# Optimization experiments

Hardware: AMD Instinct MI355X
Metric: run time of the kernel (lower is better)

The kernel has to match this reference:

```python
import jax, jax.numpy as jnp
import numpy as np

EPS = 1e-5

def conv_block(x, w, b, a, g, bt):
    # x: [B,Cin,T,F]; w: [Cout,Cin]; b: [Cout]; a: scalar PReLU slope; g,bt: [Cout,F]
    y = jnp.einsum('bctf,oc->botf', x, w) + b[None, :, None, None]
    y = jnp.maximum(y, 0.0) + a * jnp.minimum(y, 0.0)  # PReLU (single shared slope)
    mu = jnp.mean(y, axis=(1, 3), keepdims=True)
    var = jnp.var(y, axis=(1, 3), keepdims=True)       # unbiased=False
    y = (y - mu) / jnp.sqrt(var + EPS)
    return y * g[None, :, None, :] + bt[None, :, None, :]

# vmap over heads: weights have leading head axis, x is shared
_head_block = jax.vmap(conv_block, in_axes=(None, 0, 0, 0, 0, 0))


def setup_inputs() -> dict:
    key = jax.random.key(0)
    B, C, T, F = 8, 64, 1024, 64
    H, HID = 4, 4
    DV = C // H
    ks = jax.random.split(key, 16)
    s = 1.0 / np.sqrt(C)
    inp = {
        'x': jax.random.normal(ks[0], (B, C, T, F), jnp.float32),
        # per-head Q conv blocks
        'qw': jax.random.normal(ks[1], (H, HID, C), jnp.float32) * s,
        'qb': jax.random.normal(ks[2], (H, HID), jnp.float32) * 0.01,
        'qa': jnp.full((H,), 0.25, jnp.float32),
        'qg': jnp.ones((H, HID, F), jnp.float32),
        'qbeta': jnp.zeros((H, HID, F), jnp.float32),
        # per-head K conv blocks
        'kw': jax.random.normal(ks[3], (H, HID, C), jnp.float32) * s,
        'kb': jax.random.normal(ks[4], (H, HID), jnp.float32) * 0.01,
        'ka': jnp.full((H,), 0.25, jnp.float32),
        'kg': jnp.ones((H, HID, F), jnp.float32),
        'kbeta': jnp.zeros((H, HID, F), jnp.float32),
        # per-head V conv blocks (out = C//H)
        'vw': jax.random.normal(ks[5], (H, DV, C), jnp.float32) * s,
        'vb': jax.random.normal(ks[6], (H, DV), jnp.float32) * 0.01,
        'va': jnp.full((H,), 0.25, jnp.float32),
        'vg': jnp.ones((H, DV, F), jnp.float32),
        'vbeta': jnp.zeros((H, DV, F), jnp.float32),
        # final 'likear' conv block
        'lw': jax.random.normal(ks[7], (C, C), jnp.float32) * s,
        'lb': jax.random.normal(ks[8], (C,), jnp.float32) * 0.01,
        'la': jnp.float32(0.25),
        'lg': jnp.ones((C, F), jnp.float32),
        'lbeta': jnp.zeros((C, F), jnp.float32),
    }
    return inp


def reference(x, qw, qb, qa, qg, qbeta, kw, kb, ka, kg, kbeta,
              vw, vb, va, vg, vbeta, lw, lb, la, lg, lbeta):
    B, C, T, F = x.shape
    H = qw.shape[0]
    HID = qw.shape[1]
    DV = C // H
    embed = H * F  # embed_size = num_heads * num_freqs

    Q = _head_block(x, qw, qb, qa, qg, qbeta)  # [H,B,HID,T,F]
    K = _head_block(x, kw, kb, ka, kg, kbeta)  # [H,B,HID,T,F]
    V = _head_block(x, vw, vb, va, vg, vbeta)  # [H,B,DV,T,F]

    # cat over dim 0 == head-major reshape; transpose(1,2)+flatten(2)
    Ql = Q.reshape(H * B, HID, T, F).transpose(0, 2, 1, 3).reshape(H * B, T, HID * F)
    Kl = K.reshape(H * B, HID, T, F).transpose(0, 2, 1, 3).reshape(H * B, T, HID * F)
    Vl = V.reshape(H * B, DV, T, F).transpose(0, 2, 1, 3).reshape(H * B, T, DV * F)

    scores = jnp.einsum('ntd,nsd->nts', Ql, Kl) / jnp.sqrt(jnp.float32(embed))
    attn = jax.nn.softmax(scores, axis=-1)               # [HB,T,T]
    A = jnp.einsum('nts,nsd->ntd', attn, Vl)             # [HB,T,DV*F]

    A = A.reshape(H * B, T, DV, F).transpose(0, 2, 1, 3)  # [HB,DV,T,F]
    A = A.reshape(H, B, DV, T, F).transpose(1, 0, 2, 3, 4).reshape(B, C, T, F)

    out = conv_block(A, lw, lb, la, lg, lbeta)
    return out + x
```

## Files before the change

kernel.cpp:

```cpp
#include <hip/hip_runtime.h>

typedef unsigned short u16;
typedef __attribute__((ext_vector_type(8))) short short8;
typedef __attribute__((ext_vector_type(4))) float f32x4;

#define EPSV 1e-5f

__device__ __forceinline__ u16 f2bf(float f) {
    unsigned u = __float_as_uint(f);
    u += 0x7fffu + ((u >> 16) & 1u);
    return (u16)(u >> 16);
}

__device__ __forceinline__ f32x4 mfma_bf16(short8 a, short8 b, f32x4 c) {
    return __builtin_amdgcn_mfma_f32_16x16x32_bf16(a, b, c, 0, 0, 0);
}

__device__ __forceinline__ void gload_lds16(const void* g, void* l) {
    __builtin_amdgcn_global_load_lds((const __attribute__((address_space(1))) void*)g,
                                     (__attribute__((address_space(3))) void*)l, 16, 0, 0);
}

__global__ __launch_bounds__(256) void k_prep_qkv(const float* __restrict__ qw,
                                                  const float* __restrict__ kw,
                                                  const float* __restrict__ vw,
                                                  u16* __restrict__ wq)
{
    const int tid = threadIdx.x;
#pragma unroll
    for (int i = 0; i < 24; i++) {
        int idx = tid + i * 256;
        int row = idx >> 6;
        float wv = (row < 16) ? qw[idx] : ((row < 32) ? kw[idx - 1024] : vw[idx - 2048]);
        wq[idx] = f2bf(wv);
    }
}

__global__ __launch_bounds__(256) void k_prep_lw(const float* __restrict__ lw, u16* __restrict__ lwb)
{
    const int tid = threadIdx.x;
#pragma unroll
    for (int i = 0; i < 16; i++) {
        int idx = tid + i * 256;
        lwb[idx] = f2bf(lw[idx]);
    }
}

__global__ __launch_bounds__(256) void k_qkv(
    const float* __restrict__ x, const u16* __restrict__ wq,
    const float* __restrict__ qb, const float* __restrict__ qa,
    const float* __restrict__ qg, const float* __restrict__ qbt,
    const float* __restrict__ kb, const float* __restrict__ ka,
    const float* __restrict__ kg, const float* __restrict__ kbt,
    const float* __restrict__ vb, const float* __restrict__ va,
    const float* __restrict__ vg, const float* __restrict__ vbt,
    u16* __restrict__ Qb, u16* __restrict__ Kb, u16* __restrict__ Vb)
{
    __shared__ u16 xT[64][66];
    __shared__ float ys[96][66];
    __shared__ float bias_s[96], slope_s[96];

    const int tid = threadIdx.x, w = tid >> 6, lane = tid & 63;
    const int b = blockIdx.x >> 10, t = blockIdx.x & 1023;
    const int lc = lane & 15, grp = lane >> 4;

    if (tid < 96) {
        int row = tid; float bv, sv;
        if (row < 16)      { bv = qb[row];      sv = qa[row >> 2]; }
        else if (row < 32) { bv = kb[row - 16]; sv = ka[(row - 16) >> 2]; }
        else               { bv = vb[row - 32]; sv = va[(row - 32) >> 4]; }
        bias_s[row] = bv; slope_s[row] = sv;
    }
    const float* xbt = x + ((size_t)(b * 64) * 1024 + t) * 64;
#pragma unroll
    for (int k = 0; k < 4; k++) {
        int chunk = tid + k * 256;
        int c = chunk >> 4, q = chunk & 15;
        float4 v = *(const float4*)(xbt + (size_t)c * 65536 + q * 4);
        xT[q * 4 + 0][c] = f2bf(v.x);
        xT[q * 4 + 1][c] = f2bf(v.y);
        xT[q * 4 + 2][c] = f2bf(v.z);
        xT[q * 4 + 3][c] = f2bf(v.w);
    }
    __syncthreads();

#pragma unroll
    for (int i = 0; i < 6; i++) {
        int tile = w * 6 + i;
        int mt = tile >> 2, nt = tile & 3;
        f32x4 acc = {0.f, 0.f, 0.f, 0.f};
#pragma unroll
        for (int kt = 0; kt < 2; kt++) {
            short8 a  = *(const short8*)(wq + (mt * 16 + lc) * 64 + kt * 32 + grp * 8);
            short8 bf = *(const short8*)(&xT[nt * 16 + lc][kt * 32 + grp * 8]);
            acc = mfma_bf16(a, bf, acc);
        }
        int colf = nt * 16 + lc;
#pragma unroll
        for (int j = 0; j < 4; j++) {
            int row = mt * 16 + grp * 4 + j;
            float y = acc[j] + bias_s[row];
            float sl = slope_s[row];
            y = (y > 0.f) ? y : sl * y;
            ys[row][colf] = y;
        }
    }
    __syncthreads();

    const int h = w;
    {
        float v0[4]; float s = 0.f, ss = 0.f;
#pragma unroll
        for (int o = 0; o < 4; o++) { float y = ys[h * 4 + o][lane]; v0[o] = y; s += y; ss += y * y; }
#pragma unroll
        for (int m = 1; m < 64; m <<= 1) { s += __shfl_xor(s, m, 64); ss += __shfl_xor(ss, m, 64); }
        float mu = s * (1.f / 256.f), var = ss * (1.f / 256.f) - mu * mu;
        float rs = rsqrtf(var + EPSV);
        size_t base = ((size_t)(h * 8 + b) * 1024 + t) * 256;
#pragma unroll
        for (int o = 0; o < 4; o++) {
            float val = (v0[o] - mu) * rs * qg[(h * 4 + o) * 64 + lane] + qbt[(h * 4 + o) * 64 + lane];
            Qb[base + o * 64 + lane] = f2bf(val);
        }
    }
    {
        float v0[4]; float s = 0.f, ss = 0.f;
#pragma unroll
        for (int o = 0; o < 4; o++) { float y = ys[16 + h * 4 + o][lane]; v0[o] = y; s += y; ss += y * y; }
#pragma unroll
        for (int m = 1; m < 64; m <<= 1) { s += __shfl_xor(s, m, 64); ss += __shfl_xor(ss, m, 64); }
        float mu = s * (1.f / 256.f), var = ss * (1.f / 256.f) - mu * mu;
        float rs = rsqrtf(var + EPSV);
        size_t base = ((size_t)(h * 8 + b) * 1024 + t) * 256;
#pragma unroll
        for (int o = 0; o < 4; o++) {
            float val = (v0[o] - mu) * rs * kg[(h * 4 + o) * 64 + lane] + kbt[(h * 4 + o) * 64 + lane];
            Kb[base + o * 64 + lane] = f2bf(val);
        }
    }
    {
        float v0[16]; float s = 0.f, ss = 0.f;
#pragma unroll
        for (int o = 0; o < 16; o++) { float y = ys[32 + h * 16 + o][lane]; v0[o] = y; s += y; ss += y * y; }
#pragma unroll
        for (int m = 1; m < 64; m <<= 1) { s += __shfl_xor(s, m, 64); ss += __shfl_xor(ss, m, 64); }
        float mu = s * (1.f / 1024.f), var = ss * (1.f / 1024.f) - mu * mu;
        float rs = rsqrtf(var + EPSV);
        size_t base = ((size_t)(h * 8 + b) * 1024 + t) * 1024;
#pragma unroll
        for (int o = 0; o < 16; o++) {
            float val = (v0[o] - mu) * rs * vg[(h * 16 + o) * 64 + lane] + vbt[(h * 16 + o) * 64 + lane];
            Vb[base + o * 64 + lane] = f2bf(val);
        }
    }
}

__global__ __launch_bounds__(256) void k_vtrans(const u16* __restrict__ Vb, u16* __restrict__ Vt)
{
    __shared__ u16 ts[64][72];
    const int tid = threadIdx.x;
    const int idx = blockIdx.x;
    const int n = idx >> 8, rest = idx & 255;
    const int s0 = (rest >> 4) * 64, d0 = (rest & 15) * 64;
    const size_t nb = (size_t)n << 20;

#pragma unroll
    for (int i = 0; i < 2; i++) {
        int chunk = tid + i * 256;
        int row = chunk >> 3, q = chunk & 7;
        uint4 v = *(const uint4*)(Vb + nb + (size_t)(s0 + row) * 1024 + d0 + q * 8);
        *(uint4*)(&ts[row][q * 8]) = v;
    }
    __syncthreads();
#pragma unroll
    for (int i = 0; i < 2; i++) {
        int chunk = tid + i * 256;
        int orow = chunk >> 3, q = chunk & 7;
        uint4 o;
        o.x = (unsigned)ts[q * 8 + 0][orow] | ((unsigned)ts[q * 8 + 1][orow] << 16);
        o.y = (unsigned)ts[q * 8 + 2][orow] | ((unsigned)ts[q * 8 + 3][orow] << 16);
        o.z = (unsigned)ts[q * 8 + 4][orow] | ((unsigned)ts[q * 8 + 5][orow] << 16);
        o.w = (unsigned)ts[q * 8 + 6][orow] | ((unsigned)ts[q * 8 + 7][orow] << 16);
        *(uint4*)(Vt + nb + (size_t)(d0 + orow) * 1024 + s0 + q * 8) = o;
    }
}

__global__ __launch_bounds__(256) void k_attn(const u16* __restrict__ Qb, const u16* __restrict__ Kb,
                                              u16* __restrict__ P)
{
    __shared__ u16 Ks[4][16 * 256];
    __shared__ float red[2][4][16];

    const int bid = blockIdx.x;
    const int n = (bid & 7) + ((bid >> 9) << 3);
    const int qt = (bid >> 3) & 63;
    const int q0 = qt * 16;
    const int tid = threadIdx.x, w = tid >> 6, lane = tid & 63;
    const int grp = lane >> 4, lc = lane & 15;

    const u16* Qn = Qb + ((size_t)n << 18);
    const u16* Kn = Kb + ((size_t)n << 18);

    short8 qf[8];
#pragma unroll
    for (int kt = 0; kt < 8; kt++)
        qf[kt] = *(const short8*)(Qn + (size_t)(q0 + lc) * 256 + kt * 32 + grp * 8);

    u16* KsW = Ks[w];
    const int l_row = lane >> 5;
    const int l_cs = (lane & 31) * 8;

    f32x4 sacc[16];
#pragma unroll
    for (int st = 0; st < 16; st++) {
        int s0 = w * 256 + st * 16;
#pragma unroll
        for (int c = 0; c < 8; c++) {
            int row = c * 2 + l_row;
            int col = l_cs ^ ((row & 7) << 3);
            gload_lds16(Kn + (size_t)(s0 + row) * 256 + col, KsW + c * 512);
        }
        __syncthreads();
        f32x4 a = {0.f, 0.f, 0.f, 0.f};
#pragma unroll
        for (int kt = 0; kt < 8; kt++) {
            int off = lc * 256 + ((kt * 32 + grp * 8) ^ ((lc & 7) << 3));
            short8 kf = *(const short8*)(KsW + off);
            a = mfma_bf16(qf[kt], kf, a);
        }
        sacc[st] = a;
        __syncthreads();
    }

    float mx[4] = {-1e30f, -1e30f, -1e30f, -1e30f};
#pragma unroll
    for (int st = 0; st < 16; st++)
#pragma unroll
        for (int j = 0; j < 4; j++) {
            float v = sacc[st][j] * 0.0625f;
            sacc[st][j] = v;
            mx[j] = fmaxf(mx[j], v);
        }
#pragma unroll
    for (int m = 1; m < 16; m <<= 1)
#pragma unroll
        for (int j = 0; j < 4; j++) mx[j] = fmaxf(mx[j], __shfl_xor(mx[j], m, 64));

    if (lc == 0) {
#pragma unroll
        for (int j = 0; j < 4; j++) red[0][w][grp * 4 + j] = mx[j];
    }
    __syncthreads();
    float gm[4], sm[4] = {0.f, 0.f, 0.f, 0.f};
#pragma unroll
    for (int j = 0; j < 4; j++) {
        int row = grp * 4 + j;
        gm[j] = fmaxf(fmaxf(red[0][0][row], red[0][1][row]), fmaxf(red[0][2][row], red[0][3][row]));
    }
#pragma unroll
    for (int st = 0; st < 16; st++)
#pragma unroll
        for (int j = 0; j < 4; j++) {
            float p = __expf(sacc[st][j] - gm[j]);
            sacc[st][j] = p;
            sm[j] += p;
        }
#pragma unroll
    for (int m = 1; m < 16; m <<= 1)
#pragma unroll
        for (int j = 0; j < 4; j++) sm[j] += __shfl_xor(sm[j], m, 64);
    if (lc == 0) {
#pragma unroll
        for (int j = 0; j < 4; j++) red[1][w][grp * 4 + j] = sm[j];
    }
    __syncthreads();

    u16* Pn = P + ((size_t)n << 20);
    float inv[4];
#pragma unroll
    for (int j = 0; j < 4; j++) {
        int row = grp * 4 + j;
        float tot = red[1][0][row] + red[1][1][row] + red[1][2][row] + red[1][3][row];
        inv[j] = 1.f / tot;
    }
#pragma unroll
    for (int st = 0; st < 16; st++)
#pragma unroll
        for (int j = 0; j < 4; j++) {
            Pn[(size_t)(q0 + grp * 4 + j) * 1024 + w * 256 + st * 16 + lc] = f2bf(sacc[st][j] * inv[j]);
        }
}

__global__ __launch_bounds__(512, 2) void k_pv(const u16* __restrict__ P, const u16* __restrict__ Vt,
                                               float* __restrict__ out)
{
    __shared__ u16 lds[2][4][128 * 32];

    const int bid = blockIdx.x;
    const int n = (bid & 7) + ((bid >> 7) << 3);
    const int tile = (bid >> 3) & 15;
    const int tm = tile >> 2, tn = tile & 3;
    const int tid = threadIdx.x, w = tid >> 6, lane = tid & 63;
    const int wr = w >> 2, wc = w & 3;
    const int lc = lane & 15, grp = lane >> 4;

    const u16* Pa = P  + ((size_t)n << 20) + (size_t)tm * 256 * 1024;
    const u16* Va = Vt + ((size_t)n << 20) + (size_t)tn * 256 * 1024;

    const int srow = tid >> 2, scc = tid & 3;
    const int scol = (scc ^ (srow & 3)) * 8;
    const int ldst = w * 512;

    f32x4 acc[8][4];
#pragma unroll
    for (int mi = 0; mi < 8; mi++)
#pragma unroll
        for (int ni = 0; ni < 4; ni++) acc[mi][ni] = (f32x4){0.f, 0.f, 0.f, 0.f};

#define STAGE_PV(ks_, pb_)                                                        \
    {                                                                             \
        size_t k0_ = (size_t)(ks_) * 32;                                          \
        gload_lds16(Pa + (size_t)srow * 1024 + k0_ + scol,         &lds[pb_][0][ldst]); \
        gload_lds16(Pa + (size_t)(128 + srow) * 1024 + k0_ + scol, &lds[pb_][1][ldst]); \
        gload_lds16(Va + (size_t)srow * 1024 + k0_ + scol,         &lds[pb_][2][ldst]); \
        gload_lds16(Va + (size_t)(128 + srow) * 1024 + k0_ + scol, &lds[pb_][3][ldst]); \
    }

    STAGE_PV(0, 0);
    __syncthreads();

    const int rxor = (lc & 3);
    for (int ks = 0; ks < 32; ks++) {
        int cur = ks & 1;
        if (ks < 31) STAGE_PV(ks + 1, cur ^ 1);

        const u16* As = lds[cur][wr];
        const u16* Bs = lds[cur][2 + (wc >> 1)];
        const int brow0 = (wc & 1) * 64;

        short8 af[8], bf[4];
#pragma unroll
        for (int mi = 0; mi < 8; mi++)
            af[mi] = *(const short8*)(As + (mi * 16 + lc) * 32 + ((grp ^ rxor) * 8));
#pragma unroll
        for (int ni = 0; ni < 4; ni++)
            bf[ni] = *(const short8*)(Bs + (brow0 + ni * 16 + lc) * 32 + ((grp ^ rxor) * 8));

        __builtin_amdgcn_s_setprio(1);
#pragma unroll
        for (int mi = 0; mi < 8; mi++)
#pragma unroll
            for (int ni = 0; ni < 4; ni++)
                acc[mi][ni] = mfma_bf16(af[mi], bf[ni], acc[mi][ni]);
        __builtin_amdgcn_s_setprio(0);

        __syncthreads();
    }
#undef STAGE_PV

    const int h = n >> 3, b = n & 7;
#pragma unroll
    for (int mi = 0; mi < 8; mi++)
#pragma unroll
        for (int ni = 0; ni < 4; ni++) {
            int d = tn * 256 + wc * 64 + ni * 16 + lc;
            int c = h * 16 + (d >> 6), f = d & 63;
#pragma unroll
            for (int j = 0; j < 4; j++) {
                int trow = tm * 256 + wr * 128 + mi * 16 + grp * 4 + j;
                out[(((size_t)b * 64 + c) * 1024 + trow) * 64 + f] = acc[mi][ni][j];
            }
        }
}

__global__ __launch_bounds__(256) void k_final(
    const float* __restrict__ Ain, const float* __restrict__ x,
    const u16* __restrict__ lwbf, const float* __restrict__ lbias, const float* __restrict__ la,
    const float* __restrict__ lg, const float* __restrict__ lbt, float* __restrict__ out)
{
    __shared__ u16 AT[64][66];
    __shared__ float ys[64][66];
    __shared__ float red[8];

    const int tid = threadIdx.x, w = tid >> 6, lane = tid & 63;
    const int b = blockIdx.x >> 10, t = blockIdx.x & 1023;
    const int lc = lane & 15, grp = lane >> 4;

    const float* Abt = Ain + ((size_t)(b * 64) * 1024 + t) * 64;
#pragma unroll
    for (int k = 0; k < 4; k++) {
        int chunk = tid + k * 256;
        int c = chunk >> 4, q = chunk & 15;
        float4 v = *(const float4*)(Abt + (size_t)c * 65536 + q * 4);
        AT[q * 4 + 0][c] = f2bf(v.x);
        AT[q * 4 + 1][c] = f2bf(v.y);
        AT[q * 4 + 2][c] = f2bf(v.z);
        AT[q * 4 + 3][c] = f2bf(v.w);
    }
    __syncthreads();

    short8 af[2];
#pragma unroll
    for (int kt = 0; kt < 2; kt++)
        af[kt] = *(const short8*)(lwbf + (w * 16 + lc) * 64 + kt * 32 + grp * 8);

    const float slope = la[0];
    float psum = 0.f, psq = 0.f;
#pragma unroll
    for (int nt = 0; nt < 4; nt++) {
        f32x4 acc = {0.f, 0.f, 0.f, 0.f};
#pragma unroll
        for (int kt = 0; kt < 2; kt++) {
            short8 bf = *(const short8*)(&AT[nt * 16 + lc][kt * 32 + grp * 8]);
            acc = mfma_bf16(af[kt], bf, acc);
        }
#pragma unroll
        for (int j = 0; j < 4; j++) {
            int row = w * 16 + grp * 4 + j;
            float y = acc[j] + lbias[row];
            y = (y > 0.f) ? y : slope * y;
            ys[row][nt * 16 + lc] = y;
            psum += y; psq += y * y;
        }
    }
#pragma unroll
    for (int m = 1; m < 64; m <<= 1) { psum += __shfl_xor(psum, m, 64); psq += __shfl_xor(psq, m, 64); }
    if (lane == 0) { red[w] = psum; red[4 + w] = psq; }
    __syncthreads();
    float S  = red[0] + red[1] + red[2] + red[3];
    float SS = red[4] + red[5] + red[6] + red[7];
    float mu = S * (1.f / 4096.f), var = SS * (1.f / 4096.f) - mu * mu;
    float rs = rsqrtf(var + EPSV);

    for (int idx = tid; idx < 4096; idx += 256) {
        int o = idx >> 6, f = idx & 63;
        size_t gi = ((size_t)(b * 64 + o) * 1024 + t) * 64 + f;
        out[gi] = (ys[o][f] - mu) * rs * lg[idx] + lbt[idx] + x[gi];
    }
}

extern "C" void kernel_launch(void* const* d_in, const int* in_sizes, int n_in,
                              void* d_out, int out_size, void* d_ws, size_t ws_size,
                              hipStream_t stream)
{
    const float* x    = (const float*)d_in[0];
    const float* qw   = (const float*)d_in[1];
    const float* qb   = (const float*)d_in[2];
    const float* qa   = (const float*)d_in[3];
    const float* qg   = (const float*)d_in[4];
    const float* qbt  = (const float*)d_in[5];
    const float* kw   = (const float*)d_in[6];
    const float* kb   = (const float*)d_in[7];
    const float* ka   = (const float*)d_in[8];
    const float* kg   = (const float*)d_in[9];
    const float* kbt  = (const float*)d_in[10];
    const float* vw   = (const float*)d_in[11];
    const float* vb   = (const float*)d_in[12];
    const float* va   = (const float*)d_in[13];
    const float* vg   = (const float*)d_in[14];
    const float* vbt  = (const float*)d_in[15];
    const float* lw   = (const float*)d_in[16];
    const float* lb   = (const float*)d_in[17];
    const float* la   = (const float*)d_in[18];
    const float* lg   = (const float*)d_in[19];
    const float* lbt  = (const float*)d_in[20];

    float* out = (float*)d_out;

    u16* Vb = (u16*)d_ws;
    u16* Vt = (u16*)((char*)d_ws + ((size_t)64 << 20));
    u16* P  = Vb;
    u16* Qb = (u16*)d_out;
    u16* Kb = (u16*)((char*)d_out + ((size_t)16 << 20));
    u16* wqkv = Vt;

    const size_t need = ((size_t)128 << 20) + 65536;
    bool early = ws_size >= need;
    u16* lwbf = early ? (u16*)((char*)d_ws + ((ws_size - 8192) & ~(size_t)255))
                      : (u16*)d_ws;

    k_prep_qkv<<<dim3(1), dim3(256), 0, stream>>>(qw, kw, vw, wqkv);
    if (early) k_prep_lw<<<dim3(1), dim3(256), 0, stream>>>(lw, lwbf);
    k_qkv<<<dim3(8192), dim3(256), 0, stream>>>(x, wqkv, qb, qa, qg, qbt,
                                                kb, ka, kg, kbt,
                                                vb, va, vg, vbt, Qb, Kb, Vb);
    k_vtrans<<<dim3(8192), dim3(256), 0, stream>>>(Vb, Vt);
    k_attn<<<dim3(2048), dim3(256), 0, stream>>>(Qb, Kb, P);
    k_pv<<<dim3(512), dim3(512), 0, stream>>>(P, Vt, out);
    if (!early) k_prep_lw<<<dim3(1), dim3(256), 0, stream>>>(lw, lwbf);
    k_final<<<dim3(8192), dim3(256), 0, stream>>>(out, x, lwbf, lb, la, lg, lbt, out);
}
```

Measured before the change: 336.9 us.

## Process four time steps per block in QKV and final conv kernels

The QKV projection and final conv kernels now handle four time steps per block, one per wave. Each wave keeps its MFMA results in registers and does PReLU and LayerNorm there, so the ys shared-memory round trip and a barrier go away. Gamma and beta are pre-packed into bf16 pairs and staged in shared memory. This cuts grid size and reuses weight loads across more work, at the cost of more registers and LDS per block, and it lowers the precision of the affine parameters to bf16.

```diff
diff --git a/kernel.cpp b/kernel.cpp
--- a/kernel.cpp
+++ b/kernel.cpp
@@ -1,6 +1,7 @@
 #include <hip/hip_runtime.h>
 
 typedef unsigned short u16;
+typedef unsigned int u32;
 typedef __attribute__((ext_vector_type(8))) short short8;
 typedef __attribute__((ext_vector_type(4))) float f32x4;
 
@@ -21,10 +22,16 @@
                                      (__attribute__((address_space(3))) void*)l, 16, 0, 0);
 }
 
-__global__ __launch_bounds__(256) void k_prep_qkv(const float* __restrict__ qw,
-                                                  const float* __restrict__ kw,
-                                                  const float* __restrict__ vw,
-                                                  u16* __restrict__ wq)
+__device__ __forceinline__ u32 packgb(float g, float bt) {
+    return (u32)f2bf(g) | ((u32)f2bf(bt) << 16);
+}
+
+__global__ __launch_bounds__(256) void k_prep_qkv(
+    const float* __restrict__ qw, const float* __restrict__ kw, const float* __restrict__ vw,
+    const float* __restrict__ qg, const float* __restrict__ qbt,
+    const float* __restrict__ kg, const float* __restrict__ kbt,
+    const float* __restrict__ vg, const float* __restrict__ vbt,
+    u16* __restrict__ wq, u32* __restrict__ qgb)
 {
     const int tid = threadIdx.x;
 #pragma unroll
@@ -34,34 +41,45 @@
         float wv = (row < 16) ? qw[idx] : ((row < 32) ? kw[idx - 1024] : vw[idx - 2048]);
         wq[idx] = f2bf(wv);
     }
-}
-
-__global__ __launch_bounds__(256) void k_prep_lw(const float* __restrict__ lw, u16* __restrict__ lwb)
+#pragma unroll
+    for (int i = 0; i < 24; i++) {
+        int idx = tid + i * 256;
+        int row = idx >> 6;
+        float g, bt;
+        if (row < 16)      { g = qg[idx];        bt = qbt[idx]; }
+        else if (row < 32) { g = kg[idx - 1024]; bt = kbt[idx - 1024]; }
+        else               { g = vg[idx - 2048]; bt = vbt[idx - 2048]; }
+        qgb[idx] = packgb(g, bt);
+    }
+}
+
+__global__ __launch_bounds__(256) void k_prep_l(
+    const float* __restrict__ lw, const float* __restrict__ lg, const float* __restrict__ lbt,
+    u16* __restrict__ lwb, u32* __restrict__ lgb)
 {
     const int tid = threadIdx.x;
 #pragma unroll
     for (int i = 0; i < 16; i++) {
         int idx = tid + i * 256;
         lwb[idx] = f2bf(lw[idx]);
-    }
-}
-
-__global__ __launch_bounds__(256) void k_qkv(
-    const float* __restrict__ x, const u16* __restrict__ wq,
+        lgb[idx] = packgb(lg[idx], lbt[idx]);
+    }
+}
+
+__global__ __launch_bounds__(256, 2) void k_qkv(
+    const float* __restrict__ x, const u16* __restrict__ wq, const u32* __restrict__ qgb,
     const float* __restrict__ qb, const float* __restrict__ qa,
-    const float* __restrict__ qg, const float* __restrict__ qbt,
     const float* __restrict__ kb, const float* __restrict__ ka,
-    const float* __restrict__ kg, const float* __restrict__ kbt,
     const float* __restrict__ vb, const float* __restrict__ va,
-    const float* __restrict__ vg, const float* __restrict__ vbt,
     u16* __restrict__ Qb, u16* __restrict__ Kb, u16* __restrict__ Vb)
 {
-    __shared__ u16 xT[64][66];
-    __shared__ float ys[96][66];
+    __shared__ u16 xT[256][66];
+    __shared__ u32 gb_s[96][66];
     __shared__ float bias_s[96], slope_s[96];
 
     const int tid = threadIdx.x, w = tid >> 6, lane = tid & 63;
-    const int b = blockIdx.x >> 10, t = blockIdx.x & 1023;
+    const int b = blockIdx.x >> 8, tb = blockIdx.x & 255;
+    const int t0 = tb * 4, t = t0 + w;
     const int lc = lane & 15, grp = lane >> 4;
 
     if (tid < 96) {
@@ -71,87 +89,119 @@
         else               { bv = vb[row - 32]; sv = va[(row - 32) >> 4]; }
         bias_s[row] = bv; slope_s[row] = sv;
     }
-    const float* xbt = x + ((size_t)(b * 64) * 1024 + t) * 64;
-#pragma unroll
-    for (int k = 0; k < 4; k++) {
-        int chunk = tid + k * 256;
-        int c = chunk >> 4, q = chunk & 15;
-        float4 v = *(const float4*)(xbt + (size_t)c * 65536 + q * 4);
-        xT[q * 4 + 0][c] = f2bf(v.x);
-        xT[q * 4 + 1][c] = f2bf(v.y);
-        xT[q * 4 + 2][c] = f2bf(v.z);
-        xT[q * 4 + 3][c] = f2bf(v.w);
+#pragma unroll
+    for (int i = 0; i < 24; i++) {
+        int idx = tid + i * 256;
+        gb_s[idx >> 6][idx & 63] = qgb[idx];
+    }
+#pragma unroll
+    for (int k = 0; k < 16; k++) {
+        int idx = k * 256 + tid;
+        int q = idx & 15, c = (idx >> 4) & 63, tl = idx >> 10;
+        float4 v = *(const float4*)(x + ((size_t)(b * 64 + c) * 1024 + t0 + tl) * 64 + q * 4);
+        int n = tl * 64 + q * 4;
+        xT[n + 0][c] = f2bf(v.x);
+        xT[n + 1][c] = f2bf(v.y);
+        xT[n + 2][c] = f2bf(v.z);
+        xT[n + 3][c] = f2bf(v.w);
     }
     __syncthreads();
 
-#pragma unroll
-    for (int i = 0; i < 6; i++) {
-        int tile = w * 6 + i;
-        int mt = tile >> 2, nt = tile & 3;
-        f32x4 acc = {0.f, 0.f, 0.f, 0.f};
-#pragma unroll
-        for (int kt = 0; kt < 2; kt++) {
-            short8 a  = *(const short8*)(wq + (mt * 16 + lc) * 64 + kt * 32 + grp * 8);
-            short8 bf = *(const short8*)(&xT[nt * 16 + lc][kt * 32 + grp * 8]);
-            acc = mfma_bf16(a, bf, acc);
-        }
-        int colf = nt * 16 + lc;
-#pragma unroll
-        for (int j = 0; j < 4; j++) {
-            int row = mt * 16 + grp * 4 + j;
-            float y = acc[j] + bias_s[row];
-            float sl = slope_s[row];
-            y = (y > 0.f) ? y : sl * y;
-            ys[row][colf] = y;
-        }
-    }
-    __syncthreads();
-
-    const int h = w;
+    short8 bfr[4][2];
+#pragma unroll
+    for (int nt = 0; nt < 4; nt++)
+#pragma unroll
+        for (int kt = 0; kt < 2; kt++)
+            bfr[nt][kt] = *(const short8*)(&xT[w * 64 + nt * 16 + lc][kt * 32 + grp * 8]);
+
+    f32x4 acc[6][4];
+#pragma unroll
+    for (int mt = 0; mt < 6; mt++) {
+        short8 af[2];
+#pragma unroll
+        for (int kt = 0; kt < 2; kt++)
+            af[kt] = *(const short8*)(wq + (mt * 16 + lc) * 64 + kt * 32 + grp * 8);
+#pragma unroll
+        for (int nt = 0; nt < 4; nt++) {
+            f32x4 a = {0.f, 0.f, 0.f, 0.f};
+            a = mfma_bf16(af[0], bfr[nt][0], a);
+            a = mfma_bf16(af[1], bfr[nt][1], a);
+            acc[mt][nt] = a;
+        }
+    }
+
+#pragma unroll
+    for (int mt = 0; mt < 6; mt++)
+#pragma unroll
+        for (int nt = 0; nt < 4; nt++)
+#pragma unroll
+            for (int j = 0; j < 4; j++) {
+                int row = mt * 16 + grp * 4 + j;
+                float y = acc[mt][nt][j] + bias_s[row];
+                acc[mt][nt][j] = (y > 0.f) ? y : slope_s[row] * y;
+            }
+
     {
-        float v0[4]; float s = 0.f, ss = 0.f;
-#pragma unroll
-        for (int o = 0; o < 4; o++) { float y = ys[h * 4 + o][lane]; v0[o] = y; s += y; ss += y * y; }
-#pragma unroll
-        for (int m = 1; m < 64; m <<= 1) { s += __shfl_xor(s, m, 64); ss += __shfl_xor(ss, m, 64); }
+        float s = 0.f, ss = 0.f;
+#pragma unroll
+        for (int nt = 0; nt < 4; nt++)
+#pragma unroll
+            for (int j = 0; j < 4; j++) { float y = acc[0][nt][j]; s += y; ss += y * y; }
+#pragma unroll
+        for (int m = 1; m < 16; m <<= 1) { s += __shfl_xor(s, m, 64); ss += __shfl_xor(ss, m, 64); }
         float mu = s * (1.f / 256.f), var = ss * (1.f / 256.f) - mu * mu;
         float rs = rsqrtf(var + EPSV);
-        size_t base = ((size_t)(h * 8 + b) * 1024 + t) * 256;
-#pragma unroll
-        for (int o = 0; o < 4; o++) {
-            float val = (v0[o] - mu) * rs * qg[(h * 4 + o) * 64 + lane] + qbt[(h * 4 + o) * 64 + lane];
-            Qb[base + o * 64 + lane] = f2bf(val);
-        }
+        size_t base = ((size_t)(grp * 8 + b) * 1024 + t) * 256;
+#pragma unroll
+        for (int nt = 0; nt < 4; nt++)
+#pragma unroll
+            for (int j = 0; j < 4; j++) {
+                u32 p = gb_s[grp * 4 + j][nt * 16 + lc];
+                float g = __uint_as_float(p << 16), bt = __uint_as_float(p & 0xffff0000u);
+                Qb[base + j * 64 + nt * 16 + lc] = f2bf((acc[0][nt][j] - mu) * rs * g + bt);
+            }
     }
     {
-        float v0[4]; float s = 0.f, ss = 0.f;
-#pragma unroll
-        for (int o = 0; o < 4; o++) { float y = ys[16 + h * 4 + o][lane]; v0[o] = y; s += y; ss += y * y; }
-#pragma unroll
-        for (int m = 1; m < 64; m <<= 1) { s += __shfl_xor(s, m, 64); ss += __shfl_xor(ss, m, 64); }
+        float s = 0.f, ss = 0.f;
+#pragma unroll
+        for (int nt = 0; nt < 4; nt++)
+#pragma unroll
+            for (int j = 0; j < 4; j++) { float y = acc[1][nt][j]; s += y; ss += y * y; }
+#pragma unroll
+        for (int m = 1; m < 16; m <<= 1) { s += __shfl_xor(s, m, 64); ss += __shfl_xor(ss, m, 64); }
         float mu = s * (1.f / 256.f), var = ss * (1.f / 256.f) - mu * mu;
         float rs = rsqrtf(var + EPSV);
-        size_t base = ((size_t)(h * 8 + b) * 1024 + t) * 256;
-#pragma unroll
-        for (int o = 0; o < 4; o++) {
-            float val = (v0[o] - mu) * rs * kg[(h * 4 + o) * 64 + lane] + kbt[(h * 4 + o) * 64 + lane];
-            Kb[base + o * 64 + lane] = f2bf(val);
-        }
-    }
-    {
-        float v0[16]; float s = 0.f, ss = 0.f;
-#pragma unroll
-        for (int o = 0; o < 16; o++) { float y = ys[32 + h * 16 + o][lane]; v0[o] = y; s += y; ss += y * y; }
+        size_t base = ((size_t)(grp * 8 + b) * 1024 + t) * 256;
+#pragma unroll
+        for (int nt = 0; nt < 4; nt++)
+#pragma unroll
+            for (int j = 0; j < 4; j++) {
+                u32 p = gb_s[16 + grp * 4 + j][nt * 16 + lc];
+                float g = __uint_as_float(p << 16), bt = __uint_as_float(p & 0xffff0000u);
+                Kb[base + j * 64 + nt * 16 + lc] = f2bf((acc[1][nt][j] - mu) * rs * g + bt);
+            }
+    }
+#pragma unroll
+    for (int hv = 0; hv < 4; hv++) {
+        float s = 0.f, ss = 0.f;
+#pragma unroll
+        for (int nt = 0; nt < 4; nt++)
+#pragma unroll
+            for (int j = 0; j < 4; j++) { float y = acc[2 + hv][nt][j]; s += y; ss += y * y; }
 #pragma unroll
         for (int m = 1; m < 64; m <<= 1) { s += __shfl_xor(s, m, 64); ss += __shfl_xor(ss, m, 64); }
         float mu = s * (1.f / 1024.f), var = ss * (1.f / 1024.f) - mu * mu;
         float rs = rsqrtf(var + EPSV);
-        size_t base = ((size_t)(h * 8 + b) * 1024 + t) * 1024;
-#pragma unroll
-        for (int o = 0; o < 16; o++) {
-            float val = (v0[o] - mu) * rs * vg[(h * 16 + o) * 64 + lane] + vbt[(h * 16 + o) * 64 + lane];
-            Vb[base + o * 64 + lane] = f2bf(val);
-        }
+        size_t base = ((size_t)(hv * 8 + b) * 1024 + t) * 1024;
+#pragma unroll
+        for (int nt = 0; nt < 4; nt++)
+#pragma unroll
+            for (int j = 0; j < 4; j++) {
+                u32 p = gb_s[32 + hv * 16 + grp * 4 + j][nt * 16 + lc];
+                float g = __uint_as_float(p << 16), bt = __uint_as_float(p & 0xffff0000u);
+                Vb[base + (grp * 4 + j) * 64 + nt * 16 + lc] =
+                    f2bf((acc[2 + hv][nt][j] - mu) * rs * g + bt);
+            }
     }
 }
 
@@ -373,70 +423,93 @@
         }
 }
 
-__global__ __launch_bounds__(256) void k_final(
+__global__ __launch_bounds__(256, 2) void k_final(
     const float* __restrict__ Ain, const float* __restrict__ x,
-    const u16* __restrict__ lwbf, const float* __restrict__ lbias, const float* __restrict__ la,
-    const float* __restrict__ lg, const float* __restrict__ lbt, float* __restrict__ out)
-{
-    __shared__ u16 AT[64][66];
-    __shared__ float ys[64][66];
-    __shared__ float red[8];
+    const u16* __restrict__ lwbf, const u32* __restrict__ lgb,
+    const float* __restrict__ lbias, const float* __restrict__ la,
+    float* __restrict__ out)
+{
+    __shared__ u16 AT[256][66];
+    __shared__ u32 gb_s[64][66];
+    __shared__ float bias_s[64];
 
     const int tid = threadIdx.x, w = tid >> 6, lane = tid & 63;
-    const int b = blockIdx.x >> 10, t = blockIdx.x & 1023;
+    const int b = blockIdx.x >> 8, tb = blockIdx.x & 255;
+    const int t0 = tb * 4, t = t0 + w;
     const int lc = lane & 15, grp = lane >> 4;
 
-    const float* Abt = Ain + ((size_t)(b * 64) * 1024 + t) * 64;
-#pragma unroll
-    for (int k = 0; k < 4; k++) {
-        int chunk = tid + k * 256;
-        int c = chunk >> 4, q = chunk & 15;
-        float4 v = *(const float4*)(Abt + (size_t)c * 65536 + q * 4);
-        AT[q * 4 + 0][c] = f2bf(v.x);
-        AT[q * 4 + 1][c] = f2bf(v.y);
-        AT[q * 4 + 2][c] = f2bf(v.z);
-        AT[q * 4 + 3][c] = f2bf(v.w);
+    if (tid < 64) bias_s[tid] = lbias[tid];
+#pragma unroll
+    for (int i = 0; i < 16; i++) {
+        int idx = tid + i * 256;
+        gb_s[idx >> 6][idx & 63] = lgb[idx];
+    }
+#pragma unroll
+    for (int k = 0; k < 16; k++) {
+        int idx = k * 256 + tid;
+        int q = idx & 15, c = (idx >> 4) & 63, tl = idx >> 10;
+        float4 v = *(const float4*)(Ain + ((size_t)(b * 64 + c) * 1024 + t0 + tl) * 64 + q * 4);
+        int n = tl * 64 + q * 4;
+        AT[n + 0][c] = f2bf(v.x);
+        AT[n + 1][c] = f2bf(v.y);
+        AT[n + 2][c] = f2bf(v.z);
+        AT[n + 3][c] = f2bf(v.w);
     }
     __syncthreads();
 
-    short8 af[2];
-#pragma unroll
-    for (int kt = 0; kt < 2; kt++)
-        af[kt] = *(const short8*)(lwbf + (w * 16 + lc) * 64 + kt * 32 + grp * 8);
+    short8 bfr[4][2];
+#pragma unroll
+    for (int nt = 0; nt < 4; nt++)
+#pragma unroll
+        for (int kt = 0; kt < 2; kt++)
+            bfr[nt][kt] = *(const short8*)(&AT[w * 64 + nt * 16 + lc][kt * 32 + grp * 8]);
+
+    f32x4 acc[4][4];
+#pragma unroll
+    for (int mt = 0; mt < 4; mt++) {
+        short8 af[2];
+#pragma unroll
+        for (int kt = 0; kt < 2; kt++)
+            af[kt] = *(const short8*)(lwbf + (mt * 16 + lc) * 64 + kt * 32 + grp * 8);
+#pragma unroll
+        for (int nt = 0; nt < 4; nt++) {
+            f32x4 a = {0.f, 0.f, 0.f, 0.f};
+            a = mfma_bf16(af[0], bfr[nt][0], a);
+            a = mfma_bf16(af[1], bfr[nt][1], a);
+            acc[mt][nt] = a;
+        }
+    }
 
     const float slope = la[0];
-    float psum = 0.f, psq = 0.f;
-#pragma unroll
-    for (int nt = 0; nt < 4; nt++) {
-        f32x4 acc = {0.f, 0.f, 0.f, 0.f};
-#pragma unroll
-        for (int kt = 0; kt < 2; kt++) {
-            short8 bf = *(const short8*)(&AT[nt * 16 + lc][kt * 32 + grp * 8]);
-            acc = mfma_bf16(af[kt], bf, acc);
-        }
-#pragma unroll
-        for (int j = 0; j < 4; j++) {
-            int row = w * 16 + grp * 4 + j;
-            float y = acc[j] + lbias[row];
-            y = (y > 0.f) ? y : slope * y;
-            ys[row][nt * 16 + lc] = y;
-            psum += y; psq += y * y;
-        }
-    }
-#pragma unroll
-    for (int m = 1; m < 64; m <<= 1) { psum += __shfl_xor(psum, m, 64); psq += __shfl_xor(psq, m, 64); }
-    if (lane == 0) { red[w] = psum; red[4 + w] = psq; }
-    __syncthreads();
-    float S  = red[0] + red[1] + red[2] + red[3];
-    float SS = red[4] + red[5] + red[6] + red[7];
-    float mu = S * (1.f / 4096.f), var = SS * (1.f / 4096.f) - mu * mu;
+    float s = 0.f, ss = 0.f;
+#pragma unroll
+    for (int mt = 0; mt < 4; mt++)
+#pragma unroll
+        for (int nt = 0; nt < 4; nt++)
+#pragma unroll
+            for (int j = 0; j < 4; j++) {
+                float y = acc[mt][nt][j] + bias_s[mt * 16 + grp * 4 + j];
+                y = (y > 0.f) ? y : slope * y;
+                acc[mt][nt][j] = y;
+                s += y; ss += y * y;
+            }
+#pragma unroll
+    for (int m = 1; m < 64; m <<= 1) { s += __shfl_xor(s, m, 64); ss += __shfl_xor(ss, m, 64); }
+    float mu = s * (1.f / 4096.f), var = ss * (1.f / 4096.f) - mu * mu;
     float rs = rsqrtf(var + EPSV);
 
-    for (int idx = tid; idx < 4096; idx += 256) {
-        int o = idx >> 6, f = idx & 63;
-        size_t gi = ((size_t)(b * 64 + o) * 1024 + t) * 64 + f;
-        out[gi] = (ys[o][f] - mu) * rs * lg[idx] + lbt[idx] + x[gi];
-    }
+#pragma unroll
+    for (int mt = 0; mt < 4; mt++)
+#pragma unroll
+        for (int nt = 0; nt < 4; nt++)
+#pragma unroll
+            for (int j = 0; j < 4; j++) {
+                int row = mt * 16 + grp * 4 + j, f = nt * 16 + lc;
+                u32 p = gb_s[row][f];
+                float g = __uint_as_float(p << 16), bt = __uint_as_float(p & 0xffff0000u);
+                size_t gi = ((size_t)(b * 64 + row) * 1024 + t) * 64 + f;
+                out[gi] = (acc[mt][nt][j] - mu) * rs * g + bt + x[gi];
+            }
 }
 
 extern "C" void kernel_launch(void* const* d_in, const int* in_sizes, int n_in,
@@ -472,21 +545,19 @@
     u16* P  = Vb;
     u16* Qb = (u16*)d_out;
     u16* Kb = (u16*)((char*)d_out + ((size_t)16 << 20));
+
     u16* wqkv = Vt;
-
-    const size_t need = ((size_t)128 << 20) + 65536;
-    bool early = ws_size >= need;
-    u16* lwbf = early ? (u16*)((char*)d_ws + ((ws_size - 8192) & ~(size_t)255))
-                      : (u16*)d_ws;
-
-    k_prep_qkv<<<dim3(1), dim3(256), 0, stream>>>(qw, kw, vw, wqkv);
-    if (early) k_prep_lw<<<dim3(1), dim3(256), 0, stream>>>(lw, lwbf);
-    k_qkv<<<dim3(8192), dim3(256), 0, stream>>>(x, wqkv, qb, qa, qg, qbt,
-                                                kb, ka, kg, kbt,
-                                                vb, va, vg, vbt, Qb, Kb, Vb);
+    u32* qgb  = (u32*)(Vt + 8192);
+    u16* lwb  = (u16*)d_ws;
+    u32* lgb  = (u32*)((char*)d_ws + 8192);
+
+    k_prep_qkv<<<dim3(1), dim3(256), 0, stream>>>(qw, kw, vw, qg, qbt, kg, kbt, vg, vbt,
+                                                  wqkv, qgb);
+    k_qkv<<<dim3(2048), dim3(256), 0, stream>>>(x, wqkv, qgb, qb, qa, kb, ka, vb, va,
+                                                Qb, Kb, Vb);
     k_vtrans<<<dim3(8192), dim3(256), 0, stream>>>(Vb, Vt);
     k_attn<<<dim3(2048), dim3(256), 0, stream>>>(Qb, Kb, P);
     k_pv<<<dim3(512), dim3(512), 0, stream>>>(P, Vt, out);
-    if (!early) k_prep_lw<<<dim3(1), dim3(256), 0, stream>>>(lw, lwbf);
-    k_final<<<dim3(8192), dim3(256), 0, stream>>>(out, x, lwbf, lb, la, lg, lbt, out);
-}
+    k_prep_l<<<dim3(1), dim3(256), 0, stream>>>(lw, lg, lbt, lwb, lgb);
+    k_final<<<dim3(2048), dim3(256), 0, stream>>>(out, x, lwb, lgb, lb, la, out);
+}
```

Measured after the change: 324.1 us. 1.04x faster.

## Retile final conv block to four time steps per block, one wave each

Applied to the files above, without the earlier changes.

The final conv/PReLU/norm kernel now handles four consecutive time steps per block, one per wave. Each wave computes the full 64x64 output tile in registers and does its mean/variance reduction with wave shuffles, which removes the cross-wave LDS reduction and its barrier. Loading four time steps per channel makes the reads of the attention output more contiguous. Gamma and beta are packed to bf16 pairs in a prep kernel and staged in LDS, which costs some precision on those parameters. The store pattern becomes 16-lane segments per row, which may coalesce less well than the old layout.

```diff
diff --git a/kernel.cpp b/kernel.cpp
--- a/kernel.cpp
+++ b/kernel.cpp
@@ -1,6 +1,7 @@
 #include <hip/hip_runtime.h>
 
 typedef unsigned short u16;
+typedef unsigned int u32;
 typedef __attribute__((ext_vector_type(8))) short short8;
 typedef __attribute__((ext_vector_type(4))) float f32x4;
 
@@ -21,10 +22,13 @@
                                      (__attribute__((address_space(3))) void*)l, 16, 0, 0);
 }
 
-__global__ __launch_bounds__(256) void k_prep_qkv(const float* __restrict__ qw,
-                                                  const float* __restrict__ kw,
-                                                  const float* __restrict__ vw,
-                                                  u16* __restrict__ wq)
+__device__ __forceinline__ u32 packgb(float g, float bt) {
+    return (u32)f2bf(g) | ((u32)f2bf(bt) << 16);
+}
+
+__global__ __launch_bounds__(256) void k_prep_qkv(
+    const float* __restrict__ qw, const float* __restrict__ kw, const float* __restrict__ vw,
+    u16* __restrict__ wq)
 {
     const int tid = threadIdx.x;
 #pragma unroll
@@ -36,13 +40,16 @@
     }
 }
 
-__global__ __launch_bounds__(256) void k_prep_lw(const float* __restrict__ lw, u16* __restrict__ lwb)
+__global__ __launch_bounds__(256) void k_prep_l(
+    const float* __restrict__ lw, const float* __restrict__ lg, const float* __restrict__ lbt,
+    u16* __restrict__ lwb, u32* __restrict__ lgb)
 {
     const int tid = threadIdx.x;
 #pragma unroll
     for (int i = 0; i < 16; i++) {
         int idx = tid + i * 256;
         lwb[idx] = f2bf(lw[idx]);
+        lgb[idx] = packgb(lg[idx], lbt[idx]);
     }
 }
 
@@ -373,70 +380,93 @@
         }
 }
 
-__global__ __launch_bounds__(256) void k_final(
+__global__ __launch_bounds__(256, 2) void k_final(
     const float* __restrict__ Ain, const float* __restrict__ x,
-    const u16* __restrict__ lwbf, const float* __restrict__ lbias, const float* __restrict__ la,
-    const float* __restrict__ lg, const float* __restrict__ lbt, float* __restrict__ out)
-{
-    __shared__ u16 AT[64][66];
-    __shared__ float ys[64][66];
-    __shared__ float red[8];
+    const u16* __restrict__ lwbf, const u32* __restrict__ lgb,
+    const float* __restrict__ lbias, const float* __restrict__ la,
+    float* __restrict__ out)
+{
+    __shared__ u16 AT[256][66];
+    __shared__ u32 gb_s[64][66];
+    __shared__ float bias_s[64];
 
     const int tid = threadIdx.x, w = tid >> 6, lane = tid & 63;
-    const int b = blockIdx.x >> 10, t = blockIdx.x & 1023;
+    const int b = blockIdx.x >> 8, tb = blockIdx.x & 255;
+    const int t0 = tb * 4, t = t0 + w;
     const int lc = lane & 15, grp = lane >> 4;
 
-    const float* Abt = Ain + ((size_t)(b * 64) * 1024 + t) * 64;
-#pragma unroll
-    for (int k = 0; k < 4; k++) {
-        int chunk = tid + k * 256;
-        int c = chunk >> 4, q = chunk & 15;
-        float4 v = *(const float4*)(Abt + (size_t)c * 65536 + q * 4);
-        AT[q * 4 + 0][c] = f2bf(v.x);
-        AT[q * 4 + 1][c] = f2bf(v.y);
-        AT[q * 4 + 2][c] = f2bf(v.z);
-        AT[q * 4 + 3][c] = f2bf(v.w);
-    }
-    __syncthreads();
-
-    short8 af[2];
-#pragma unroll
-    for (int kt = 0; kt < 2; kt++)
-        af[kt] = *(const short8*)(lwbf + (w * 16 + lc) * 64 + kt * 32 + grp * 8);
+    if (tid < 64) bias_s[tid] = lbias[tid];
+#pragma unroll
+    for (int i = 0; i < 16; i++) {
+        int idx = tid + i * 256;
+        gb_s[idx >> 6][idx & 63] = lgb[idx];
+    }
+#pragma unroll
+    for (int k = 0; k < 16; k++) {
+        int idx = k * 256 + tid;
+        int q = idx & 15, c = (idx >> 4) & 63, tl = idx >> 10;
+        float4 v = *(const float4*)(Ain + ((size_t)(b * 64 + c) * 1024 + t0 + tl) * 64 + q * 4);
+        int n = tl * 64 + q * 4;
+        AT[n + 0][c] = f2bf(v.x);
+        AT[n + 1][c] = f2bf(v.y);
+        AT[n + 2][c] = f2bf(v.z);
+        AT[n + 3][c] = f2bf(v.w);
+    }
+    __syncthreads();
+
+    short8 bfr[4][2];
+#pragma unroll
+    for (int nt = 0; nt < 4; nt++)
+#pragma unroll
+        for (int kt = 0; kt < 2; kt++)
+            bfr[nt][kt] = *(const short8*)(&AT[w * 64 + nt * 16 + lc][kt * 32 + grp * 8]);
+
+    f32x4 acc[4][4];
+#pragma unroll
+    for (int mt = 0; mt < 4; mt++) {
+        short8 af[2];
+#pragma unroll
+        for (int kt = 0; kt < 2; kt++)
+            af[kt] = *(const short8*)(lwbf + (mt * 16 + lc) * 64 + kt * 32 + grp * 8);
+#pragma unroll
+        for (int nt = 0; nt < 4; nt++) {
+            f32x4 a = {0.f, 0.f, 0.f, 0.f};
+            a = mfma_bf16(af[0], bfr[nt][0], a);
+            a = mfma_bf16(af[1], bfr[nt][1], a);
+            acc[mt][nt] = a;
+        }
+    }
 
     const float slope = la[0];
-    float psum = 0.f, psq = 0.f;
-#pragma unroll
-    for (int nt = 0; nt < 4; nt++) {
-        f32x4 acc = {0.f, 0.f, 0.f, 0.f};
-#pragma unroll
-        for (int kt = 0; kt < 2; kt++) {
-            short8 bf = *(const short8*)(&AT[nt * 16 + lc][kt * 32 + grp * 8]);
-            acc = mfma_bf16(af[kt], bf, acc);
-        }
-#pragma unroll
-        for (int j = 0; j < 4; j++) {
-            int row = w * 16 + grp * 4 + j;
-            float y = acc[j] + lbias[row];
-            y = (y > 0.f) ? y : slope * y;
-            ys[row][nt * 16 + lc] = y;
-            psum += y; psq += y * y;
-        }
-    }
-#pragma unroll
-    for (int m = 1; m < 64; m <<= 1) { psum += __shfl_xor(psum, m, 64); psq += __shfl_xor(psq, m, 64); }
-    if (lane == 0) { red[w] = psum; red[4 + w] = psq; }
-    __syncthreads();
-    float S  = red[0] + red[1] + red[2] + red[3];
-    float SS = red[4] + red[5] + red[6] + red[7];
-    float mu = S * (1.f / 4096.f), var = SS * (1.f / 4096.f) - mu * mu;
+    float s = 0.f, ss = 0.f;
+#pragma unroll
+    for (int mt = 0; mt < 4; mt++)
+#pragma unroll
+        for (int nt = 0; nt < 4; nt++)
+#pragma unroll
+            for (int j = 0; j < 4; j++) {
+                float y = acc[mt][nt][j] + bias_s[mt * 16 + grp * 4 + j];
+                y = (y > 0.f) ? y : slope * y;
+                acc[mt][nt][j] = y;
+                s += y; ss += y * y;
+            }
+#pragma unroll
+    for (int m = 1; m < 64; m <<= 1) { s += __shfl_xor(s, m, 64); ss += __shfl_xor(ss, m, 64); }
+    float mu = s * (1.f / 4096.f), var = ss * (1.f / 4096.f) - mu * mu;
     float rs = rsqrtf(var + EPSV);
 
-    for (int idx = tid; idx < 4096; idx += 256) {
-        int o = idx >> 6, f = idx & 63;
-        size_t gi = ((size_t)(b * 64 + o) * 1024 + t) * 64 + f;
-        out[gi] = (ys[o][f] - mu) * rs * lg[idx] + lbt[idx] + x[gi];
-    }
+#pragma unroll
+    for (int mt = 0; mt < 4; mt++)
+#pragma unroll
+        for (int nt = 0; nt < 4; nt++)
+#pragma unroll
+            for (int j = 0; j < 4; j++) {
+                int row = mt * 16 + grp * 4 + j, f = nt * 16 + lc;
+                u32 p = gb_s[row][f];
+                float g = __uint_as_float(p << 16), bt = __uint_as_float(p & 0xffff0000u);
+                size_t gi = ((size_t)(b * 64 + row) * 1024 + t) * 64 + f;
+                out[gi] = (acc[mt][nt][j] - mu) * rs * g + bt + x[gi];
+            }
 }
 
 extern "C" void kernel_launch(void* const* d_in, const int* in_sizes, int n_in,
@@ -472,21 +502,18 @@
     u16* P  = Vb;
     u16* Qb = (u16*)d_out;
     u16* Kb = (u16*)((char*)d_out + ((size_t)16 << 20));
+
     u16* wqkv = Vt;
-
-    const size_t need = ((size_t)128 << 20) + 65536;
-    bool early = ws_size >= need;
-    u16* lwbf = early ? (u16*)((char*)d_ws + ((ws_size - 8192) & ~(size_t)255))
-                      : (u16*)d_ws;
+    u16* lwb  = (u16*)d_ws;
+    u32* lgb  = (u32*)((char*)d_ws + 8192);
 
     k_prep_qkv<<<dim3(1), dim3(256), 0, stream>>>(qw, kw, vw, wqkv);
-    if (early) k_prep_lw<<<dim3(1), dim3(256), 0, stream>>>(lw, lwbf);
     k_qkv<<<dim3(8192), dim3(256), 0, stream>>>(x, wqkv, qb, qa, qg, qbt,
                                                 kb, ka, kg, kbt,
                                                 vb, va, vg, vbt, Qb, Kb, Vb);
     k_vtrans<<<dim3(8192), dim3(256), 0, stream>>>(Vb, Vt);
     k_attn<<<dim3(2048), dim3(256), 0, stream>>>(Qb, Kb, P);
     k_pv<<<dim3(512), dim3(512), 0, stream>>>(P, Vt, out);
-    if (!early) k_prep_lw<<<dim3(1), dim3(256), 0, stream>>>(lw, lwbf);
-    k_final<<<dim3(8192), dim3(256), 0, stream>>>(out, x, lwbf, lb, la, lg, lbt, out);
-}
+    k_prep_l<<<dim3(1), dim3(256), 0, stream>>>(lw, lg, lbt, lwb, lgb);
+    k_final<<<dim3(2048), dim3(256), 0, stream>>>(out, x, lwb, lgb, lb, la, out);
+}
```

Result: no change. 331.6 us (-1.6%).
